# Optimization experiments

Measured on AMD Instinct MI355X. Metric: run time of the kernel, lower is better.

## Reference

```python
import jax, jax.numpy as jnp
import numpy as np

SUB_NO, T_NO, T_DATA, E_NO, I_NO, N_BASIS = 20, 200, 50000, 2000, 500, 20


def _make_cos_basis():
    x = np.arange(T_NO, dtype=np.float32)
    raw = 6.0 * np.log(x + 1.0)  # cos_scale=6, cos_shift=1
    basis = np.zeros((N_BASIS, T_NO), np.float32)
    for i in range(N_BASIS):
        phi = 0.5 * np.pi * i
        b = 0.5 * np.cos(raw - phi) + 0.5
        basis[i] = np.where((raw < phi - np.pi) | (raw > phi + np.pi), 0.0, b)
    return basis


def _make_tree():
    C = np.zeros((SUB_NO, SUB_NO), np.int32)
    for p in range(SUB_NO):
        for c in (2 * p + 1, 2 * p + 2):
            if c < SUB_NO:
                C[p, c] = 1
    return C


def _one_hot_assign(n_syn):
    C = np.zeros((SUB_NO, n_syn), np.int32)
    C[np.arange(n_syn) % SUB_NO, np.arange(n_syn)] = 1
    return C


def setup_inputs() -> dict:
    key = jax.random.key(0)
    ks = jax.random.split(key, 12)
    f32 = jnp.float32
    S_e = (jax.random.uniform(ks[0], (T_DATA, E_NO)) < 0.02).astype(f32)
    S_i = (jax.random.uniform(ks[1], (T_DATA, I_NO)) < 0.02).astype(f32)
    Z = (jax.random.uniform(ks[2], (T_DATA,)) < 0.05).astype(f32)
    return {
        "S_e": S_e, "S_i": S_i, "Z": Z,
        "C_den": jnp.asarray(_make_tree()),
        "C_syn_e": jnp.asarray(_one_hot_assign(E_NO)),
        "C_syn_i": jnp.asarray(_one_hot_assign(I_NO)),
        "cos_basis": jnp.asarray(_make_cos_basis()),
        "W_syn": jax.random.normal(ks[3], (SUB_NO, N_BASIS, 2), f32) * 0.1,
        "W_hist": jax.random.normal(ks[4], (N_BASIS,), f32) * 0.1,
        "W_sub": jnp.ones((SUB_NO,), f32) * 0.1,
        "W_spk": jnp.ones((1,), f32),
        "Tau_spk": jnp.ones((1,), f32) * 3.0,
        "V_o": jax.random.normal(ks[5], (1,), f32),
        "Theta": jax.random.normal(ks[6], (SUB_NO,), f32) * 0.1,
        "weight1": jax.random.normal(ks[7], (SUB_NO, 5), f32) * 0.1,
        "weight2": jax.random.normal(ks[8], (SUB_NO, 5, 5), f32) * 0.1,
        "weight3": jax.random.normal(ks[9], (SUB_NO, 5, 5), f32) * 0.1,
        "weight4": jax.random.normal(ks[10], (5, SUB_NO), f32) * 0.1,
    }


def reference(S_e, S_i, Z, C_den, C_syn_e, C_syn_i, cos_basis, W_syn, W_hist,
              W_sub, W_spk, Tau_spk, V_o, Theta, weight1, weight2, weight3, weight4):
    f32 = jnp.float32
    T = S_e.shape[0]
    sub_no = weight1.shape[0]
    T_no = cos_basis.shape[1]
    Cd = C_den.astype(f32)

    # synapse -> subunit projection
    syn_e = S_e @ C_syn_e.astype(f32).T  # [T, sub]
    syn_i = S_i @ C_syn_i.astype(f32).T

    e_kern = W_syn[:, :, 0] @ cos_basis  # [sub, T_no]
    i_kern = W_syn[:, :, 1] @ cos_basis

    def grouped_causal_conv(x, kern):
        # torch: pad T_no-1 zeros in front, grouped conv with flipped kernel (true causal conv)
        xp = jnp.pad(x, ((T_no - 1, 0), (0, 0))).T[None]  # [1, sub, T+T_no-1]
        k = kern[:, None, ::-1]  # [sub, 1, T_no]
        y = jax.lax.conv_general_dilated(xp, k, (1,), 'VALID',
                                         dimension_numbers=('NCH', 'OIH', 'NCH'),
                                         feature_group_count=x.shape[1])
        return y[0].T  # [T, sub]

    syn = grouped_causal_conv(syn_e, e_kern) + grouped_causal_conv(syn_i, i_kern)

    def causal_conv_lag1(z, kern):
        # torch: pad T_no zeros in front, valid conv with flipped kernel, drop last -> [T]
        zp = jnp.pad(z, (T_no, 0))[None, None]  # [1,1,T+T_no]
        k = kern[None, None, ::-1]
        y = jax.lax.conv_general_dilated(zp, k, (1,), 'VALID',
                                         dimension_numbers=('NCH', 'OIH', 'NCH'))
        return y[0, 0, :-1]

    hist_kern = W_hist @ cos_basis  # [T_no]
    hist_filt = causal_conv_lag1(Z, hist_kern)

    lrelu = jax.nn.leaky_relu  # negative_slope 0.01 matches torch default
    W_sub2 = W_sub ** 2

    def sub_mlp(s, x):
        h = lrelu(x[:, None] * weight1[s][None, :])  # [T,5]
        h = lrelu(h @ weight2[s])
        h = lrelu(h @ weight3[s])
        return h @ weight4[:, s]  # [T]

    # tree recurrence: children have higher index, processed last-to-first
    ns_out = jnp.zeros((T, sub_no), f32)
    for s in range(sub_no - 1):
        sub_idx = sub_no - 1 - s
        agg = ns_out @ (Cd[sub_idx] * W_sub2)  # equals gather-leaf weighted sum (0 if leaf)
        ns_in = lrelu(syn[:, sub_idx] + Theta[sub_idx] + agg)
        ns_out = ns_out.at[:, sub_idx].set(sub_mlp(sub_idx, ns_in))

    root_in = lrelu(hist_filt + syn[:, 0] + ns_out @ (Cd[0] * W_sub2) + Theta[0])
    final_Z = jax.nn.sigmoid(sub_mlp(0, root_in))

    t = jnp.arange(T_no, dtype=f32)
    t_tau = t / Tau_spk[0] ** 2
    spk_kern = t_tau * jnp.exp(-t_tau) * W_spk[0] ** 2
    final_V = causal_conv_lag1(Z, spk_kern) + V_o[0]

    out_filters = jnp.concatenate([e_kern, i_kern, hist_kern[None, :]], axis=0)
    return final_V, final_Z, out_filters
```

## Files before the change

kernel.cpp:

```cpp
#include <hip/hip_runtime.h>
#include <math.h>

#define T_DATA 50000
#define T_NO 200
#define N_BASIS 20

#define WS_E    0
#define WS_I    1000000
#define WS_EKT  2000000
#define WS_IKT  2004000
#define WS_WSE  2008400
#define WS_HF   2008800

#define KA_ROWS_PB 12
#define KA_RED_BLOCKS 4167
#define KA_HIST_BLOCKS 196
#define KA_TOTAL (KA_RED_BLOCKS + KA_HIST_BLOCKS + 1)

__device__ __forceinline__ float lrelu(float x) { return x > 0.f ? x : 0.01f * x; }

__global__ __launch_bounds__(256) void kA(const float* __restrict__ Se,
                                          const float* __restrict__ Si,
                                          const float* __restrict__ Z,
                                          const int* __restrict__ C_den,
                                          const float* __restrict__ cb,
                                          const float* __restrict__ W_syn,
                                          const float* __restrict__ W_hist,
                                          const float* __restrict__ W_sub,
                                          const float* __restrict__ W_spk,
                                          const float* __restrict__ Tau,
                                          const float* __restrict__ Vo,
                                          float* __restrict__ ws,
                                          float* __restrict__ out) {
    int tid = threadIdx.x;
    int bid = blockIdx.x;

    if (bid < KA_RED_BLOCKS) {
        __shared__ float4 ldsE[KA_ROWS_PB * 20];
        __shared__ float4 ldsI[KA_ROWS_PB * 20];
        int t_loc = tid / 20, sg = tid % 20;
        int t = bid * KA_ROWS_PB + t_loc;
        bool act = (tid < KA_ROWS_PB * 20) && (t < T_DATA);
        const float4* Se4 = (const float4*)Se;
        const float4* Si4 = (const float4*)Si;

        float4 aE = make_float4(0.f, 0.f, 0.f, 0.f);
        float4 aI = make_float4(0.f, 0.f, 0.f, 0.f);
        if (act) {
            const float4* rowE = Se4 + (long)t * 500;
            #pragma unroll
            for (int k = 0; k < 25; k++) {
                float4 v = rowE[sg + 20 * k];
                aE.x += v.x; aE.y += v.y; aE.z += v.z; aE.w += v.w;
            }
            const float4* rowI = Si4 + (long)t * 125;
            #pragma unroll
            for (int k = 0; k < 7; k++) {
                int f = sg + 20 * k;
                if (f < 125) {
                    float4 v = rowI[f];
                    aI.x += v.x; aI.y += v.y; aI.z += v.z; aI.w += v.w;
                }
            }
        }
        if (tid < KA_ROWS_PB * 20) {
            ldsE[tid] = aE;
            ldsI[tid] = aI;
        }
        __syncthreads();
        if (tid < KA_ROWS_PB * 5) {
            int tl = tid / 5, r = tid % 5;
            float4 sE = make_float4(0.f, 0.f, 0.f, 0.f);
            float4 sI = make_float4(0.f, 0.f, 0.f, 0.f);
            #pragma unroll
            for (int m = 0; m < 4; m++) {
                float4 vE = ldsE[tl * 20 + r + 5 * m];
                float4 vI = ldsI[tl * 20 + r + 5 * m];
                sE.x += vE.x; sE.y += vE.y; sE.z += vE.z; sE.w += vE.w;
                sI.x += vI.x; sI.y += vI.y; sI.z += vI.z; sI.w += vI.w;
            }
            int tt = bid * KA_ROWS_PB + tl;
            if (tt < T_DATA) {
                ((float4*)(ws + WS_E))[tt * 5 + r] = sE;
                ((float4*)(ws + WS_I))[tt * 5 + r] = sI;
            }
        }
        return;
    }

    if (bid < KA_RED_BLOCKS + KA_HIST_BLOCKS) {
        __shared__ float z[456];
        __shared__ float2 hk[200];
        int t0 = (bid - KA_RED_BLOCKS) * 256;
        for (int f = tid; f < 456; f += 256) {
            int u = t0 - 200 + f;
            z[f] = (u >= 0 && u < T_DATA) ? Z[u] : 0.f;
        }
        if (tid < 200) {
            float h = 0.f;
            #pragma unroll
            for (int b = 0; b < N_BASIS; b++) h += W_hist[b] * cb[b * 200 + tid];
            float tau2 = Tau[0] * Tau[0];
            float tt = (float)tid / tau2;
            float sk = tt * expf(-tt) * W_spk[0] * W_spk[0];
            hk[tid] = make_float2(h, sk);
        }
        __syncthreads();
        float ha = 0.f, sa = 0.f;
        #pragma unroll 4
        for (int tau = 0; tau < T_NO; tau++) {
            float zv = z[tid + 199 - tau];
            float2 hv = hk[tau];
            ha += zv * hv.x;
            sa += zv * hv.y;
        }
        int t = t0 + tid;
        if (t < T_DATA) {
            out[t] = sa + Vo[0];
            ws[WS_HF + t] = ha;
        }
        return;
    }

    for (int j = tid; j < 4000; j += 256) {
        int s = j / 200, tau = j % 200;
        float se = 0.f, si = 0.f;
        #pragma unroll
        for (int b = 0; b < N_BASIS; b++) {
            float c = cb[b * 200 + tau];
            se += W_syn[(s * N_BASIS + b) * 2 + 0] * c;
            si += W_syn[(s * N_BASIS + b) * 2 + 1] * c;
        }
        ws[WS_EKT + tau * 20 + s] = se;
        ws[WS_IKT + tau * 20 + s] = si;
        out[2 * T_DATA + j] = se;
        out[2 * T_DATA + 4000 + j] = si;
    }
    for (int j = tid; j < 200; j += 256) {
        float h = 0.f;
        #pragma unroll
        for (int b = 0; b < N_BASIS; b++) h += W_hist[b] * cb[b * 200 + j];
        out[2 * T_DATA + 8000 + j] = h;
    }
    for (int j = tid; j < 400; j += 256) {
        int c = j % 20;
        ws[WS_WSE + j] = (float)C_den[j] * W_sub[c] * W_sub[c];
    }
}

__device__ __forceinline__ float sub_mlp(int s, float x,
                                         const float* __restrict__ w1,
                                         const float* __restrict__ w2,
                                         const float* __restrict__ w3,
                                         const float* __restrict__ w4) {
    float h1[5], h2[5], h3[5];
    #pragma unroll
    for (int k = 0; k < 5; k++) h1[k] = lrelu(x * w1[s * 5 + k]);
    #pragma unroll
    for (int j = 0; j < 5; j++) {
        float v = 0.f;
        #pragma unroll
        for (int k = 0; k < 5; k++) v += h1[k] * w2[s * 25 + k * 5 + j];
        h2[j] = lrelu(v);
    }
    #pragma unroll
    for (int j = 0; j < 5; j++) {
        float v = 0.f;
        #pragma unroll
        for (int k = 0; k < 5; k++) v += h2[k] * w3[s * 25 + k * 5 + j];
        h3[j] = lrelu(v);
    }
    float o = 0.f;
    #pragma unroll
    for (int k = 0; k < 5; k++) o += h3[k] * w4[k * 20 + s];
    return o;
}

#define KB_X 64
#define KB_T 256
#define KB_ROWS 455
#define KB_SRP 115
#define KB_THREADS 640

__global__ __launch_bounds__(KB_THREADS) void kB(const float* __restrict__ ws,
                                                 const float* __restrict__ Theta,
                                                 const float* __restrict__ w1,
                                                 const float* __restrict__ w2,
                                                 const float* __restrict__ w3,
                                                 const float* __restrict__ w4,
                                                 float* __restrict__ out) {
    __shared__ float4 tile[2 * 5 * 4 * KB_SRP];
    int x = threadIdx.x;
    int sg = __builtin_amdgcn_readfirstlane(threadIdx.y);
    int z  = __builtin_amdgcn_readfirstlane(threadIdx.z);
    int t0 = blockIdx.x * KB_T;
    int lin = x + 64 * sg + 320 * z;

    const float4* wsE4 = (const float4*)(ws + WS_E);
    const float4* wsI4 = (const float4*)(ws + WS_I);
    long gbase = (long)(t0 - 199) * 5;
    for (int f = lin; f < KB_ROWS * 5; f += KB_THREADS) {
        long g = gbase + f;
        int row = f / 5, gg = f % 5;
        int sub = row & 3, idx = row >> 2;
        float4 ve = make_float4(0.f, 0.f, 0.f, 0.f);
        float4 vi = ve;
        if (g >= 0 && g < (long)T_DATA * 5) {
            ve = wsE4[g];
            vi = wsI4[g];
        }
        tile[((0 * 5 + gg) * 4 + sub) * KB_SRP + idx] = ve;
        tile[((1 * 5 + gg) * 4 + sub) * KB_SRP + idx] = vi;
    }
    __syncthreads();

    const float4* eK = (const float4*)(ws + WS_EKT);
    const float4* iK = (const float4*)(ws + WS_IKT);
    const float4* te = &tile[(0 * 5 + sg) * 4 * KB_SRP];
    const float4* ti = &tile[(1 * 5 + sg) * 4 * KB_SRP];

    float4 we[4], wi[4], acc[4];
    #pragma unroll
    for (int j = 0; j < 4; j++) acc[j] = make_float4(0.f, 0.f, 0.f, 0.f);
    int idx0 = x + 50 - 25 * z;
    we[0] = te[0 * KB_SRP + idx0]; wi[0] = ti[0 * KB_SRP + idx0];
    we[1] = te[1 * KB_SRP + idx0]; wi[1] = ti[1 * KB_SRP + idx0];
    we[2] = te[2 * KB_SRP + idx0]; wi[2] = ti[2 * KB_SRP + idx0];

    int m0 = 25 * z;
    for (int mm = 0; mm < 25; mm++) {
        int m = m0 + mm;
        int idx = x + 49 - m;
        #pragma unroll
        for (int p = 0; p < 4; p++) {
            int tau = 4 * m + p;
            const int s0 = (3 - p) & 3;
            we[s0] = te[s0 * KB_SRP + idx];
            wi[s0] = ti[s0 * KB_SRP + idx];
            float4 ke = eK[tau * 5 + sg];
            float4 ki = iK[tau * 5 + sg];
            #pragma unroll
            for (int j = 0; j < 4; j++) {
                const int sl = (s0 + j) & 3;
                acc[j].x += we[sl].x * ke.x + wi[sl].x * ki.x;
                acc[j].y += we[sl].y * ke.y + wi[sl].y * ki.y;
                acc[j].z += we[sl].z * ke.z + wi[sl].z * ki.z;
                acc[j].w += we[sl].w * ke.w + wi[sl].w * ki.w;
            }
        }
    }

    __syncthreads();
    float4* accP = tile;
    #pragma unroll
    for (int j = 0; j < 4; j++) accP[((z * 20) + sg * 4 + j) * 64 + x] = acc[j];
    __syncthreads();

    if (lin >= 256) return;
    int w = lin >> 6, xr = lin & 63;
    int t = t0 + 4 * xr + w;
    if (t >= T_DATA) return;

    float acc20[20];
    #pragma unroll
    for (int g = 0; g < 5; g++) {
        float4 v0 = accP[(g * 4 + w) * 64 + xr];
        float4 v1 = accP[(20 + g * 4 + w) * 64 + xr];
        acc20[g * 4 + 0] = v0.x + v1.x; acc20[g * 4 + 1] = v0.y + v1.y;
        acc20[g * 4 + 2] = v0.z + v1.z; acc20[g * 4 + 3] = v0.w + v1.w;
    }
    const float* wse = ws + WS_WSE;
    float ns[20];
    #pragma unroll
    for (int s = 0; s < 20; s++) ns[s] = 0.f;
    #pragma unroll
    for (int si = 19; si >= 1; si--) {
        float ag = 0.f;
        #pragma unroll
        for (int c = 0; c < 20; c++) ag += wse[si * 20 + c] * ns[c];
        float xx = lrelu(acc20[si] + Theta[si] + ag);
        ns[si] = sub_mlp(si, xx, w1, w2, w3, w4);
    }
    float ag0 = 0.f;
    #pragma unroll
    for (int c = 0; c < 20; c++) ag0 += wse[c] * ns[c];
    float x0 = lrelu(ws[WS_HF + t] + acc20[0] + ag0 + Theta[0]);
    float zf = sub_mlp(0, x0, w1, w2, w3, w4);
    out[T_DATA + t] = 1.f / (1.f + expf(-zf));
}

extern "C" void kernel_launch(void* const* d_in, const int* in_sizes, int n_in,
                              void* d_out, int out_size, void* d_ws, size_t ws_size,
                              hipStream_t stream) {
    const float* S_e    = (const float*)d_in[0];
    const float* S_i    = (const float*)d_in[1];
    const float* Z      = (const float*)d_in[2];
    const int*   C_den  = (const int*)d_in[3];
    const float* cb     = (const float*)d_in[6];
    const float* W_syn  = (const float*)d_in[7];
    const float* W_hist = (const float*)d_in[8];
    const float* W_sub  = (const float*)d_in[9];
    const float* W_spk  = (const float*)d_in[10];
    const float* Tau    = (const float*)d_in[11];
    const float* V_o    = (const float*)d_in[12];
    const float* Theta  = (const float*)d_in[13];
    const float* w1     = (const float*)d_in[14];
    const float* w2     = (const float*)d_in[15];
    const float* w3     = (const float*)d_in[16];
    const float* w4     = (const float*)d_in[17];
    float* out = (float*)d_out;
    float* ws  = (float*)d_ws;

    kA<<<KA_TOTAL, 256, 0, stream>>>(S_e, S_i, Z, C_den, cb, W_syn, W_hist,
                                     W_sub, W_spk, Tau, V_o, ws, out);
    dim3 b3(KB_X, 5, 2);
    kB<<<(T_DATA + KB_T - 1) / KB_T, b3, 0, stream>>>(
        ws, Theta, w1, w2, w3, w4, out);
}
```

Measured before the change: 663.1 us.

## Stage spike rows through LDS with coalesced loads before per-subunit reduction

The synaptic reduction kernel now has each block copy 4 full rows of S_e and S_i into shared memory with fully coalesced, contiguous float4 loads. It then reduces them from LDS in three partial chunks per row, followed by a final combine. The previous version had each thread stride through global memory 20 float4s apart. The aim is better global memory coalescing on this dominant bandwidth-bound pass, at the cost of more blocks, a larger LDS footprint (about 40KB per block, which limits occupancy), and an extra synchronisation.

Result: slower. 677.7 us (+2.2%).

```diff
diff --git a/kernel.cpp b/kernel.cpp
--- a/kernel.cpp
+++ b/kernel.cpp
@@ -12,8 +12,10 @@
 #define WS_WSE  2008400
 #define WS_HF   2008800
 
-#define KA_ROWS_PB 12
-#define KA_RED_BLOCKS 4167
+#define RB_ROWS 4
+#define STRIDE_E 501
+#define STRIDE_I 126
+#define KA_RED_BLOCKS 12500
 #define KA_HIST_BLOCKS 196
 #define KA_TOTAL (KA_RED_BLOCKS + KA_HIST_BLOCKS + 1)
 
@@ -35,66 +37,92 @@
     int tid = threadIdx.x;
     int bid = blockIdx.x;
 
+    __shared__ float4 ldsE[RB_ROWS * STRIDE_E];
+    __shared__ float4 ldsI[RB_ROWS * STRIDE_I];
+    __shared__ float4 cE[RB_ROWS * 3 * 20];
+    __shared__ float4 cI[RB_ROWS * 20];
+    __shared__ float zsh[456];
+    __shared__ float2 hk[200];
+
     if (bid < KA_RED_BLOCKS) {
-        __shared__ float4 ldsE[KA_ROWS_PB * 20];
-        __shared__ float4 ldsI[KA_ROWS_PB * 20];
-        int t_loc = tid / 20, sg = tid % 20;
-        int t = bid * KA_ROWS_PB + t_loc;
-        bool act = (tid < KA_ROWS_PB * 20) && (t < T_DATA);
+        int t0 = bid * RB_ROWS;
         const float4* Se4 = (const float4*)Se;
         const float4* Si4 = (const float4*)Si;
 
-        float4 aE = make_float4(0.f, 0.f, 0.f, 0.f);
-        float4 aI = make_float4(0.f, 0.f, 0.f, 0.f);
-        if (act) {
-            const float4* rowE = Se4 + (long)t * 500;
-            #pragma unroll
-            for (int k = 0; k < 25; k++) {
-                float4 v = rowE[sg + 20 * k];
+        long gE = (long)t0 * 500;
+        #pragma unroll
+        for (int it = 0; it < 8; it++) {
+            int i = tid + it * 256;
+            if (i < 2000) {
+                int row = i / 500, f = i % 500;
+                ldsE[row * STRIDE_E + f] = Se4[gE + i];
+            }
+        }
+        long gI = (long)t0 * 125;
+        #pragma unroll
+        for (int it = 0; it < 2; it++) {
+            int i = tid + it * 256;
+            if (i < 500) {
+                int row = i / 125, f = i % 125;
+                ldsI[row * STRIDE_I + f] = Si4[gI + i];
+            }
+        }
+        __syncthreads();
+
+        if (tid < 240) {
+            int row = tid / 60, rem = tid % 60;
+            int sg = rem % 20, kp = rem / 20;
+            const float4* eb = &ldsE[row * STRIDE_E];
+            int k0 = (kp == 0) ? 0 : (kp == 1) ? 9 : 17;
+            int k1 = (kp == 0) ? 9 : (kp == 1) ? 17 : 25;
+            float4 aE = make_float4(0.f, 0.f, 0.f, 0.f);
+            for (int k = k0; k < k1; k++) {
+                float4 v = eb[sg + 20 * k];
                 aE.x += v.x; aE.y += v.y; aE.z += v.z; aE.w += v.w;
             }
-            const float4* rowI = Si4 + (long)t * 125;
-            #pragma unroll
-            for (int k = 0; k < 7; k++) {
-                int f = sg + 20 * k;
-                if (f < 125) {
-                    float4 v = rowI[f];
-                    aI.x += v.x; aI.y += v.y; aI.z += v.z; aI.w += v.w;
+            cE[(row * 3 + kp) * 20 + sg] = aE;
+            if (kp == 0) {
+                const float4* ib = &ldsI[row * STRIDE_I];
+                float4 aI = make_float4(0.f, 0.f, 0.f, 0.f);
+                #pragma unroll
+                for (int k = 0; k < 7; k++) {
+                    int f = sg + 20 * k;
+                    if (f < 125) {
+                        float4 v = ib[f];
+                        aI.x += v.x; aI.y += v.y; aI.z += v.z; aI.w += v.w;
+                    }
                 }
-            }
-        }
-        if (tid < KA_ROWS_PB * 20) {
-            ldsE[tid] = aE;
-            ldsI[tid] = aI;
+                cI[row * 20 + sg] = aI;
+            }
         }
         __syncthreads();
-        if (tid < KA_ROWS_PB * 5) {
-            int tl = tid / 5, r = tid % 5;
+
+        if (tid < RB_ROWS * 5) {
+            int row = tid / 5, c = tid % 5;
             float4 sE = make_float4(0.f, 0.f, 0.f, 0.f);
             float4 sI = make_float4(0.f, 0.f, 0.f, 0.f);
             #pragma unroll
             for (int m = 0; m < 4; m++) {
-                float4 vE = ldsE[tl * 20 + r + 5 * m];
-                float4 vI = ldsI[tl * 20 + r + 5 * m];
-                sE.x += vE.x; sE.y += vE.y; sE.z += vE.z; sE.w += vE.w;
-                sI.x += vI.x; sI.y += vI.y; sI.z += vI.z; sI.w += vI.w;
-            }
-            int tt = bid * KA_ROWS_PB + tl;
-            if (tt < T_DATA) {
-                ((float4*)(ws + WS_E))[tt * 5 + r] = sE;
-                ((float4*)(ws + WS_I))[tt * 5 + r] = sI;
-            }
+                int sg = c + 5 * m;
+                #pragma unroll
+                for (int kp = 0; kp < 3; kp++) {
+                    float4 v = cE[(row * 3 + kp) * 20 + sg];
+                    sE.x += v.x; sE.y += v.y; sE.z += v.z; sE.w += v.w;
+                }
+                float4 w = cI[row * 20 + sg];
+                sI.x += w.x; sI.y += w.y; sI.z += w.z; sI.w += w.w;
+            }
+            ((float4*)(ws + WS_E))[(t0 + row) * 5 + c] = sE;
+            ((float4*)(ws + WS_I))[(t0 + row) * 5 + c] = sI;
         }
         return;
     }
 
     if (bid < KA_RED_BLOCKS + KA_HIST_BLOCKS) {
-        __shared__ float z[456];
-        __shared__ float2 hk[200];
         int t0 = (bid - KA_RED_BLOCKS) * 256;
         for (int f = tid; f < 456; f += 256) {
             int u = t0 - 200 + f;
-            z[f] = (u >= 0 && u < T_DATA) ? Z[u] : 0.f;
+            zsh[f] = (u >= 0 && u < T_DATA) ? Z[u] : 0.f;
         }
         if (tid < 200) {
             float h = 0.f;
@@ -109,7 +137,7 @@
         float ha = 0.f, sa = 0.f;
         #pragma unroll 4
         for (int tau = 0; tau < T_NO; tau++) {
-            float zv = z[tid + 199 - tau];
+            float zv = zsh[tid + 199 - tau];
             float2 hv = hk[tau];
             ha += zv * hv.x;
             sa += zv * hv.y;
```
